# Optimization experiments

Hardware: AMD Instinct MI355X
Metric: run time of the kernel (lower is better)

The kernel has to match this reference:

```python
import jax, jax.numpy as jnp
import numpy as np

N_NODES = 50000
N_EDGES = 800000
DIM = 64
N_HEADS = 4


def setup_inputs() -> dict:
    key = jax.random.key(0)
    ks = jax.random.split(key, 7)
    x = jax.random.normal(ks[0], (N_NODES, DIM), dtype=jnp.float32)
    Wq = jax.random.normal(ks[1], (DIM, DIM), dtype=jnp.float32) / np.sqrt(DIM)
    Wk = jax.random.normal(ks[2], (DIM, DIM), dtype=jnp.float32) / np.sqrt(DIM)
    Wv = jax.random.normal(ks[3], (DIM, DIM), dtype=jnp.float32) / np.sqrt(DIM)
    Wo = jax.random.normal(ks[4], (DIM, DIM), dtype=jnp.float32) / np.sqrt(DIM)
    src = jax.random.randint(ks[5], (N_EDGES,), 0, N_NODES, dtype=jnp.int32)
    dst = jax.random.randint(ks[6], (N_EDGES,), 0, N_NODES, dtype=jnp.int32)
    return {"x": x, "Wq": Wq, "Wk": Wk, "Wv": Wv, "Wo": Wo, "src": src, "dst": dst}


def _scatter_softmax(scores, dst, n_nodes):
    # scores: [E, H]; per-destination-node softmax over incoming edges.
    m = jax.ops.segment_max(scores, dst, num_segments=n_nodes)  # [N, H]
    m = jnp.maximum(m, jnp.float32(-1e9))  # mirror the -1e9 init of the torch code
    ex = jnp.exp(scores - m[dst])  # [E, H]
    denom = jax.ops.segment_sum(ex, dst, num_segments=n_nodes)  # [N, H]
    return ex / (denom[dst] + 1e-9)


def reference(x, Wq, Wk, Wv, Wo, src, dst):
    N, D = x.shape
    H = N_HEADS
    Dh = D // H
    q = (x @ Wq).reshape(N, H, Dh)
    k = (x @ Wk).reshape(N, H, Dh)
    v = (x @ Wv).reshape(N, H, Dh)
    # per-edge attention logits: [E, H]
    scores = jnp.einsum("ehd,ehd->eh", q[dst], k[src]) / jnp.sqrt(jnp.float32(Dh))
    alpha = _scatter_softmax(scores, dst, N)  # [E, H]
    # weighted aggregation of source values onto destination nodes
    agg = jax.ops.segment_sum(alpha[:, :, None] * v[src], dst, num_segments=N)  # [N, H, Dh]
    return agg.reshape(N, D) @ Wo
```

## Files before the change

### kernel.cpp

```cpp
#include <hip/hip_runtime.h>
#include <math.h>

#define HEADS 4
#define DH 16
#define D 64
#define MAXDEG 64

typedef unsigned short ushort_t;
typedef unsigned int uint_t;

__device__ __forceinline__ float bf2f(ushort_t u) {
    return __uint_as_float(((uint_t)u) << 16);
}
__device__ __forceinline__ ushort_t f2bf(float f) {
    uint_t u = __float_as_uint(f);
    u = (u + 0x7FFFu + ((u >> 16) & 1u)) >> 16;
    return (ushort_t)u;
}
__device__ __forceinline__ float bflo(uint_t u) { return __uint_as_float(u << 16); }
__device__ __forceinline__ float bfhi(uint_t u) { return __uint_as_float(u & 0xFFFF0000u); }
__device__ __forceinline__ uint_t pack2(float a, float b) {
    return (uint_t)f2bf(a) | ((uint_t)f2bf(b) << 16);
}

__global__ __launch_bounds__(256) void qkv_scatter_kernel(
        const float* __restrict__ x,
        const float* __restrict__ Wq,
        const float* __restrict__ Wk,
        const float* __restrict__ Wv,
        ushort_t* __restrict__ qbf,
        ushort_t* __restrict__ kbf,
        ushort_t* __restrict__ vbf,
        const int* __restrict__ src,
        const int* __restrict__ dst,
        int* __restrict__ cursor,
        ushort_t* __restrict__ csr,
        int N, int E) {
    __shared__ ushort_t wq[D][D];
    __shared__ ushort_t wk[D][D];
    __shared__ ushort_t wv[D][D];
    __shared__ float xs[16][D];

    int tid = threadIdx.x;
    for (int i = tid; i < D * D; i += 256) {
        wq[i >> 6][i & 63] = f2bf(Wq[i]);
        wk[i >> 6][i & 63] = f2bf(Wk[i]);
        wv[i >> 6][i & 63] = f2bf(Wv[i]);
    }

    int c = tid & 63;
    int g = tid >> 6;
    int row = tid >> 4;
    int col4 = tid & 15;

    int ntiles = (N + 15) >> 4;
    for (int tile = blockIdx.x; tile < ntiles; tile += gridDim.x) {
        int n0t = tile * 16;
        __syncthreads();
        float4 xv = make_float4(0.f, 0.f, 0.f, 0.f);
        if (n0t + row < N) xv = *(const float4*)(x + (size_t)(n0t + row) * D + col4 * 4);
        *(float4*)&xs[row][col4 * 4] = xv;
        __syncthreads();

        float aq0=0,aq1=0,aq2=0,aq3=0, ak0=0,ak1=0,ak2=0,ak3=0, av0=0,av1=0,av2=0,av3=0;
#pragma unroll 8
        for (int d = 0; d < D; ++d) {
            float wqv = bf2f(wq[d][c]), wkv = bf2f(wk[d][c]), wvv = bf2f(wv[d][c]);
            float x0 = xs[g*4+0][d], x1 = xs[g*4+1][d], x2 = xs[g*4+2][d], x3 = xs[g*4+3][d];
            aq0 += x0*wqv; ak0 += x0*wkv; av0 += x0*wvv;
            aq1 += x1*wqv; ak1 += x1*wkv; av1 += x1*wvv;
            aq2 += x2*wqv; ak2 += x2*wkv; av2 += x2*wvv;
            aq3 += x3*wqv; ak3 += x3*wkv; av3 += x3*wvv;
        }
        int nb = n0t + g * 4;
        if (nb+0 < N) { qbf[(size_t)(nb+0)*D+c]=f2bf(aq0); kbf[(size_t)(nb+0)*D+c]=f2bf(ak0); vbf[(size_t)(nb+0)*D+c]=f2bf(av0); }
        if (nb+1 < N) { qbf[(size_t)(nb+1)*D+c]=f2bf(aq1); kbf[(size_t)(nb+1)*D+c]=f2bf(ak1); vbf[(size_t)(nb+1)*D+c]=f2bf(av1); }
        if (nb+2 < N) { qbf[(size_t)(nb+2)*D+c]=f2bf(aq2); kbf[(size_t)(nb+2)*D+c]=f2bf(ak2); vbf[(size_t)(nb+2)*D+c]=f2bf(av2); }
        if (nb+3 < N) { qbf[(size_t)(nb+3)*D+c]=f2bf(aq3); kbf[(size_t)(nb+3)*D+c]=f2bf(ak3); vbf[(size_t)(nb+3)*D+c]=f2bf(av3); }
    }

    {
        int e0 = (int)((long long)E * blockIdx.x / gridDim.x);
        int e1 = (int)((long long)E * (blockIdx.x + 1) / gridDim.x);
        for (int e = e0 + tid; e < e1; e += 256) {
            int d = dst[e];
            int s = src[e];
            int pos = atomicAdd(&cursor[d], 1);
            if (pos < MAXDEG) csr[(size_t)d * MAXDEG + pos] = (ushort_t)s;
        }
    }
}

__global__ __launch_bounds__(256) void attn_kernel(const ushort_t* __restrict__ qbf,
                                                   const ushort_t* __restrict__ kbf,
                                                   const ushort_t* __restrict__ vbf,
                                                   const ushort_t* __restrict__ csr,
                                                   const int* __restrict__ cursor,
                                                   ushort_t* __restrict__ aggbf,
                                                   int N) {
    int lane = threadIdx.x & 63;
    int wave = threadIdx.x >> 6;
    int node = blockIdx.x * 4 + wave;
    if (node >= N) return;

    int hp  = lane & 3;
    int el  = lane >> 2;
    int hd  = (lane & 31) >> 3;
    int par = lane >> 5;
    int dp2 = 2 * (lane & 31);

    int cnt = cursor[node]; if (cnt > MAXDEG) cnt = MAXDEG;
    const ushort_t* row = csr + (size_t)node * MAXDEG;

    float qr[16];
    {
        const uint4* qp = (const uint4*)(qbf + (size_t)node * D + hp * DH);
        uint4 qa = qp[0], qb = qp[1];
        qr[0]=bflo(qa.x);  qr[1]=bfhi(qa.x);  qr[2]=bflo(qa.y);  qr[3]=bfhi(qa.y);
        qr[4]=bflo(qa.z);  qr[5]=bfhi(qa.z);  qr[6]=bflo(qa.w);  qr[7]=bfhi(qa.w);
        qr[8]=bflo(qb.x);  qr[9]=bfhi(qb.x);  qr[10]=bflo(qb.y); qr[11]=bfhi(qb.y);
        qr[12]=bflo(qb.z); qr[13]=bfhi(qb.z); qr[14]=bflo(qb.w); qr[15]=bfhi(qb.w);
    }

    int s0=0, s1=0, s2=0, s3=0;
    float sc0=-1e30f, sc1=-1e30f, sc2=-1e30f, sc3=-1e30f;

#define PH1SB(sb, sv, scv)                                                      \
    if ((sb) * 16 < cnt) {                                                      \
        int eidx = (sb) * 16 + el;                                              \
        if (eidx < cnt) sv = row[eidx];                                         \
        const uint4* kp = (const uint4*)(kbf + (size_t)sv * D + hp * DH);       \
        uint4 ka = kp[0], kb = kp[1];                                           \
        float dot =                                                             \
          bflo(ka.x)*qr[0]  + bfhi(ka.x)*qr[1]                                  \
        + bflo(ka.y)*qr[2]  + bfhi(ka.y)*qr[3]                                  \
        + bflo(ka.z)*qr[4]  + bfhi(ka.z)*qr[5]                                  \
        + bflo(ka.w)*qr[6]  + bfhi(ka.w)*qr[7]                                  \
        + bflo(kb.x)*qr[8]  + bfhi(kb.x)*qr[9]                                  \
        + bflo(kb.y)*qr[10] + bfhi(kb.y)*qr[11]                                 \
        + bflo(kb.z)*qr[12] + bfhi(kb.z)*qr[13]                                 \
        + bflo(kb.w)*qr[14] + bfhi(kb.w)*qr[15];                                \
        scv = (eidx < cnt) ? dot * 0.25f : -1e30f;                              \
    }
    PH1SB(0, s0, sc0)
    PH1SB(1, s1, sc1)
    PH1SB(2, s2, sc2)
    PH1SB(3, s3, sc3)
#undef PH1SB

    float mloc = fmaxf(fmaxf(sc0, sc1), fmaxf(sc2, sc3));
    mloc = fmaxf(mloc, __shfl_xor(mloc, 4, 64));
    mloc = fmaxf(mloc, __shfl_xor(mloc, 8, 64));
    mloc = fmaxf(mloc, __shfl_xor(mloc, 16, 64));
    mloc = fmaxf(mloc, __shfl_xor(mloc, 32, 64));
    mloc = fmaxf(mloc, -1e9f);

    float pv0 = __expf(sc0 - mloc);
    float pv1 = __expf(sc1 - mloc);
    float pv2 = __expf(sc2 - mloc);
    float pv3 = __expf(sc3 - mloc);
    float ls = (pv0 + pv1) + (pv2 + pv3);
    ls += __shfl_xor(ls, 4, 64);
    ls += __shfl_xor(ls, 8, 64);
    ls += __shfl_xor(ls, 16, 64);
    ls += __shfl_xor(ls, 32, 64);

    float inv = 1.f / (__shfl(ls, hd, 64) + 1e-9f);

    float2 a0 = {0.f, 0.f}, a1 = {0.f, 0.f};
#define PH3SB(sb, sv, pvv)                                                      \
    if ((sb) * 16 < cnt) {                                                      \
        int lim = cnt - (sb) * 16; if (lim > 16) lim = 16;                      \
        for (int e2 = 0; e2 < lim; e2 += 4) {                                   \
            int L0 = 4 * (e2 + par);                                            \
            int ss0 = __shfl(sv, L0, 64);                                       \
            float p0 = __shfl(pvv, L0 + hd, 64);                                \
            uint_t w0 = *(const uint_t*)(vbf + (size_t)ss0 * D + dp2);          \
            a0.x += p0 * bflo(w0);                                              \
            a0.y += p0 * bfhi(w0);                                              \
            int L1 = 4 * (e2 + 2 + par);                                        \
            int ss1 = __shfl(sv, L1, 64);                                       \
            float p1 = __shfl(pvv, L1 + hd, 64);                                \
            uint_t w1 = *(const uint_t*)(vbf + (size_t)ss1 * D + dp2);          \
            a1.x += p1 * bflo(w1);                                              \
            a1.y += p1 * bfhi(w1);                                              \
        }                                                                       \
    }
    PH3SB(0, s0, pv0)
    PH3SB(1, s1, pv1)
    PH3SB(2, s2, pv2)
    PH3SB(3, s3, pv3)
#undef PH3SB

    float ax = a0.x + a1.x, ay = a0.y + a1.y;
    ax += __shfl_xor(ax, 32, 64);
    ay += __shfl_xor(ay, 32, 64);
    if (lane < 32) {
        *(uint_t*)(aggbf + (size_t)node * D + dp2) = pack2(ax * inv, ay * inv);
    }
}

__global__ __launch_bounds__(256) void out_kernel(const ushort_t* __restrict__ aggbf,
                                                  const float* __restrict__ Wo,
                                                  float* __restrict__ out, int N) {
    __shared__ float wo[D][D];
    __shared__ float xs[16][D];

    int tid = threadIdx.x;
    for (int i = tid; i < D * D; i += 256) wo[i >> 6][i & 63] = Wo[i];

    int c = tid & 63;
    int g = tid >> 6;
    int row = tid >> 4;
    int col4 = tid & 15;

    int ntiles = (N + 15) >> 4;
    for (int tile = blockIdx.x; tile < ntiles; tile += gridDim.x) {
        int n0 = tile * 16;
        __syncthreads();
        uint2 av = make_uint2(0u, 0u);
        if (n0 + row < N) av = *(const uint2*)(aggbf + (size_t)(n0 + row) * D + col4 * 4);
        xs[row][col4 * 4 + 0] = bflo(av.x);
        xs[row][col4 * 4 + 1] = bfhi(av.x);
        xs[row][col4 * 4 + 2] = bflo(av.y);
        xs[row][col4 * 4 + 3] = bfhi(av.y);
        __syncthreads();

        float a0 = 0.f, a1 = 0.f, a2 = 0.f, a3 = 0.f;
#pragma unroll 8
        for (int d = 0; d < D; ++d) {
            float w = wo[d][c];
            a0 += xs[g*4+0][d] * w;
            a1 += xs[g*4+1][d] * w;
            a2 += xs[g*4+2][d] * w;
            a3 += xs[g*4+3][d] * w;
        }
        int nb = n0 + g * 4;
        if (nb+0 < N) out[(size_t)(nb+0)*D+c] = a0;
        if (nb+1 < N) out[(size_t)(nb+1)*D+c] = a1;
        if (nb+2 < N) out[(size_t)(nb+2)*D+c] = a2;
        if (nb+3 < N) out[(size_t)(nb+3)*D+c] = a3;
    }
}

extern "C" void kernel_launch(void* const* d_in, const int* in_sizes, int n_in,
                              void* d_out, int out_size, void* d_ws, size_t ws_size,
                              hipStream_t stream) {
    const float* x  = (const float*)d_in[0];
    const float* Wq = (const float*)d_in[1];
    const float* Wk = (const float*)d_in[2];
    const float* Wv = (const float*)d_in[3];
    const float* Wo = (const float*)d_in[4];
    const int* src  = (const int*)d_in[5];
    const int* dst  = (const int*)d_in[6];
    float* out = (float*)d_out;

    int N = in_sizes[0] / D;
    int E = in_sizes[5];

    char* ws = (char*)d_ws;
    ushort_t* qbf   = (ushort_t*)ws;  ws += (size_t)N * D * 2;
    ushort_t* kbf   = (ushort_t*)ws;  ws += (size_t)N * D * 2;
    ushort_t* vbf   = (ushort_t*)ws;  ws += (size_t)N * D * 2;
    ushort_t* aggbf = (ushort_t*)ws;  ws += (size_t)N * D * 2;
    int* cursor     = (int*)ws;       ws += (size_t)N * 4;
    ushort_t* csr   = (ushort_t*)ws;  ws += (size_t)N * MAXDEG * 2;

    int nTiles16 = (N + 15) / 16;
    int gemmGrid = nTiles16 < 2048 ? nTiles16 : 2048;
    int attnGrid = (N + 3) / 4;

    hipMemsetAsync(cursor, 0, (size_t)N * 4, stream);
    qkv_scatter_kernel<<<2048, 256, 0, stream>>>(x, Wq, Wk, Wv, qbf, kbf, vbf,
                                                 src, dst, cursor, csr, N, E);
    attn_kernel<<<attnGrid, 256, 0, stream>>>(qbf, kbf, vbf, csr, cursor, aggbf, N);
    out_kernel<<<gemmGrid, 256, 0, stream>>>(aggbf, Wo, out, N);
}
```

Before: 126.1 us.

## Fuse output projection into attention kernel, drop aggregation buffer

Folds the Wo projection into the attention kernel. Each wave writes its node's aggregated vector to shared memory, then computes one output column per lane from a shared-memory copy of Wo. This removes the bf16 agg round trip through global memory and one kernel launch. In exchange, every block reloads the 16KB Wo into LDS, the block size grows to 512 threads, and the wave reads aggsh without any barrier.

```diff
diff --git a/kernel.cpp b/kernel.cpp
--- a/kernel.cpp
+++ b/kernel.cpp
@@ -19,9 +19,6 @@
 }
 __device__ __forceinline__ float bflo(uint_t u) { return __uint_as_float(u << 16); }
 __device__ __forceinline__ float bfhi(uint_t u) { return __uint_as_float(u & 0xFFFF0000u); }
-__device__ __forceinline__ uint_t pack2(float a, float b) {
-    return (uint_t)f2bf(a) | ((uint_t)f2bf(b) << 16);
-}
 
 __global__ __launch_bounds__(256) void qkv_scatter_kernel(
         const float* __restrict__ x,
@@ -91,16 +88,24 @@
     }
 }
 
-__global__ __launch_bounds__(256) void attn_kernel(const ushort_t* __restrict__ qbf,
+__global__ __launch_bounds__(512) void attn_kernel(const ushort_t* __restrict__ qbf,
                                                    const ushort_t* __restrict__ kbf,
                                                    const ushort_t* __restrict__ vbf,
                                                    const ushort_t* __restrict__ csr,
                                                    const int* __restrict__ cursor,
-                                                   ushort_t* __restrict__ aggbf,
+                                                   const float* __restrict__ Wo,
+                                                   float* __restrict__ out,
                                                    int N) {
-    int lane = threadIdx.x & 63;
-    int wave = threadIdx.x >> 6;
-    int node = blockIdx.x * 4 + wave;
+    __shared__ float wo[D][D];
+    __shared__ float aggsh[8][D];
+
+    int tid = threadIdx.x;
+    for (int i = tid; i < D * D; i += 512) wo[i >> 6][i & 63] = Wo[i];
+    __syncthreads();
+
+    int lane = tid & 63;
+    int wave = tid >> 6;
+    int node = blockIdx.x * 8 + wave;
     if (node >= N) return;
 
     int hp  = lane & 3;
@@ -196,51 +201,16 @@
     ax += __shfl_xor(ax, 32, 64);
     ay += __shfl_xor(ay, 32, 64);
     if (lane < 32) {
-        *(uint_t*)(aggbf + (size_t)node * D + dp2) = pack2(ax * inv, ay * inv);
-    }
-}
-
-__global__ __launch_bounds__(256) void out_kernel(const ushort_t* __restrict__ aggbf,
-                                                  const float* __restrict__ Wo,
-                                                  float* __restrict__ out, int N) {
-    __shared__ float wo[D][D];
-    __shared__ float xs[16][D];
-
-    int tid = threadIdx.x;
-    for (int i = tid; i < D * D; i += 256) wo[i >> 6][i & 63] = Wo[i];
-
-    int c = tid & 63;
-    int g = tid >> 6;
-    int row = tid >> 4;
-    int col4 = tid & 15;
-
-    int ntiles = (N + 15) >> 4;
-    for (int tile = blockIdx.x; tile < ntiles; tile += gridDim.x) {
-        int n0 = tile * 16;
-        __syncthreads();
-        uint2 av = make_uint2(0u, 0u);
-        if (n0 + row < N) av = *(const uint2*)(aggbf + (size_t)(n0 + row) * D + col4 * 4);
-        xs[row][col4 * 4 + 0] = bflo(av.x);
-        xs[row][col4 * 4 + 1] = bfhi(av.x);
-        xs[row][col4 * 4 + 2] = bflo(av.y);
-        xs[row][col4 * 4 + 3] = bfhi(av.y);
-        __syncthreads();
-
-        float a0 = 0.f, a1 = 0.f, a2 = 0.f, a3 = 0.f;
+        aggsh[wave][dp2]     = ax * inv;
+        aggsh[wave][dp2 + 1] = ay * inv;
+    }
+
+    float o = 0.f;
 #pragma unroll 8
-        for (int d = 0; d < D; ++d) {
-            float w = wo[d][c];
-            a0 += xs[g*4+0][d] * w;
-            a1 += xs[g*4+1][d] * w;
-            a2 += xs[g*4+2][d] * w;
-            a3 += xs[g*4+3][d] * w;
-        }
-        int nb = n0 + g * 4;
-        if (nb+0 < N) out[(size_t)(nb+0)*D+c] = a0;
-        if (nb+1 < N) out[(size_t)(nb+1)*D+c] = a1;
-        if (nb+2 < N) out[(size_t)(nb+2)*D+c] = a2;
-        if (nb+3 < N) out[(size_t)(nb+3)*D+c] = a3;
-    }
+    for (int d = 0; d < D; ++d) {
+        o += aggsh[wave][d] * wo[d][lane];
+    }
+    out[(size_t)node * D + lane] = o;
 }
 
 extern "C" void kernel_launch(void* const* d_in, const int* in_sizes, int n_in,
@@ -262,17 +232,13 @@
     ushort_t* qbf   = (ushort_t*)ws;  ws += (size_t)N * D * 2;
     ushort_t* kbf   = (ushort_t*)ws;  ws += (size_t)N * D * 2;
     ushort_t* vbf   = (ushort_t*)ws;  ws += (size_t)N * D * 2;
-    ushort_t* aggbf = (ushort_t*)ws;  ws += (size_t)N * D * 2;
     int* cursor     = (int*)ws;       ws += (size_t)N * 4;
     ushort_t* csr   = (ushort_t*)ws;  ws += (size_t)N * MAXDEG * 2;
 
-    int nTiles16 = (N + 15) / 16;
-    int gemmGrid = nTiles16 < 2048 ? nTiles16 : 2048;
-    int attnGrid = (N + 3) / 4;
+    int attnGrid = (N + 7) / 8;
 
     hipMemsetAsync(cursor, 0, (size_t)N * 4, stream);
     qkv_scatter_kernel<<<2048, 256, 0, stream>>>(x, Wq, Wk, Wv, qbf, kbf, vbf,
                                                  src, dst, cursor, csr, N, E);
-    attn_kernel<<<attnGrid, 256, 0, stream>>>(qbf, kbf, vbf, csr, cursor, aggbf, N);
-    out_kernel<<<gemmGrid, 256, 0, stream>>>(aggbf, Wo, out, N);
-}
+    attn_kernel<<<attnGrid, 512, 0, stream>>>(qbf, kbf, vbf, csr, cursor, Wo, out, N);
+}
```

After: 125.8 us. No clear change (-0.2%).
